# Optimization experiments

Hardware: AMD Instinct MI355X
Metric: run time of the kernel (lower is better)

Reference implementation:

```python
import jax, jax.numpy as jnp
import numpy as np

N = 400000
C_IN = 64
C_OUT = 64
K = 27  # 3x3x3 kernel offsets
EPS = 1e-4


def _subm_conv(feat, nbr_t, W):
    # feat: [N, Cin], nbr_t: [K, N] int32, W: [K, Cin, Cout]
    # rulebook-style gather-GEMM-scatter: accumulate over kernel offsets
    def body(acc, kw):
        Wk, idxk = kw
        return acc + feat[idxk] @ Wk, None
    init = jnp.zeros((feat.shape[0], W.shape[-1]), feat.dtype)
    out, _ = jax.lax.scan(body, init, (W, nbr_t))
    return out


def _bn(x, g, b):
    # BatchNorm1d with track_running_stats=False: always uses batch stats
    m = x.mean(axis=0)
    v = x.var(axis=0)
    return (x - m) * jax.lax.rsqrt(v + EPS) * g + b


def _lrelu(x, slope):
    return jnp.where(x >= 0, x, slope * x)


def setup_inputs() -> dict:
    key = jax.random.key(0)
    ks = jax.random.split(key, 11)
    features = jax.random.normal(ks[0], (N, C_IN), dtype=jnp.float32)
    neighbor_idx = jax.random.randint(ks[1], (N, K), 0, N, dtype=jnp.int32)
    s = 0.05
    W1 = jax.random.normal(ks[2], (K, C_IN, C_OUT), dtype=jnp.float32) * s
    W2 = jax.random.normal(ks[3], (K, C_OUT, C_OUT), dtype=jnp.float32) * s
    W3 = jax.random.normal(ks[4], (K, C_OUT, C_OUT), dtype=jnp.float32) * s
    g1 = jax.random.normal(ks[5], (C_OUT,), dtype=jnp.float32) * 0.1 + 1.0
    b1 = jax.random.normal(ks[6], (C_OUT,), dtype=jnp.float32) * 0.1
    g2 = jax.random.normal(ks[7], (C_OUT,), dtype=jnp.float32) * 0.1 + 1.0
    b2 = jax.random.normal(ks[8], (C_OUT,), dtype=jnp.float32) * 0.1
    g3 = jax.random.normal(ks[9], (C_OUT,), dtype=jnp.float32) * 0.1 + 1.0
    b3 = jax.random.normal(ks[10], (C_OUT,), dtype=jnp.float32) * 0.1
    return {"features": features, "neighbor_idx": neighbor_idx,
            "W1": W1, "g1": g1, "b1": b1,
            "W2": W2, "g2": g2, "b2": b2,
            "W3": W3, "g3": g3, "b3": b3}


def reference(features, neighbor_idx, W1, g1, b1, W2, g2, b2, W3, g3, b3):
    nbr_t = neighbor_idx.T  # [K, N]
    # conv_block1: subm conv -> BN -> LeakyReLU(0.05)
    x = _lrelu(_bn(_subm_conv(features, nbr_t, W1), g1, b1), 0.05)
    res = x
    # conv_block2
    x = _lrelu(_bn(_subm_conv(x, nbr_t, W2), g2, b2), 0.05)
    # conv_block3 (no activation) + norm
    x = _bn(_subm_conv(x, nbr_t, W3), g3, b3)
    # residual add + scn.LeakyReLU (default leakiness = 1/3)
    return _lrelu(x + res, 0.333)
```

## Files before the change

kernel.cpp:

```cpp
#include <hip/hip_runtime.h>
#include <hip/hip_bf16.h>

#define N_PTS 400000
#define KOFF 27
#define AP 72

typedef __attribute__((ext_vector_type(8))) short short8;
typedef __attribute__((ext_vector_type(4))) float float4v;

__device__ __forceinline__ unsigned short f2bf(float f) {
    union { float f; unsigned int u; } a; a.f = f;
    unsigned int u = a.u;
    unsigned int r = (u + 0x7FFFu + ((u >> 16) & 1u)) >> 16;
    return (unsigned short)r;
}

__device__ __forceinline__ float bf2f(unsigned short u) {
    union { unsigned int u; float f; } a; a.u = ((unsigned int)u) << 16;
    return a.f;
}

__global__ void cast_feat_kernel(const float* __restrict__ src,
                                 unsigned short* __restrict__ dst, int n4) {
    int i = blockIdx.x * blockDim.x + threadIdx.x;
    if (i >= n4) return;
    const float4* s4 = (const float4*)src;
    float4 v = s4[i];
    ushort4 o;
    o.x = f2bf(v.x); o.y = f2bf(v.y); o.z = f2bf(v.z); o.w = f2bf(v.w);
    ((ushort4*)dst)[i] = o;
}

__global__ void prep_w_all_kernel(const float* __restrict__ W1,
                                  const float* __restrict__ W2,
                                  const float* __restrict__ W3,
                                  unsigned short* __restrict__ Wt,
                                  float* __restrict__ stats) {
    int i = blockIdx.x * blockDim.x + threadIdx.x;
    if (i < 384) stats[i] = 0.0f;
    if (i >= KOFF * 64 * 64) return;
    int k = i >> 12;
    int co = (i >> 6) & 63;
    int ci = i & 63;
    int src = (k << 12) + (ci << 6) + co;
    const int WS = KOFF * 4096;
    Wt[i] = f2bf(W1[src]);
    Wt[i + WS] = f2bf(W2[src]);
    Wt[i + 2 * WS] = f2bf(W3[src]);
}

__global__ __launch_bounds__(512, 6)
void conv_kernel(const unsigned short* __restrict__ X,
                 const int* __restrict__ nbr,
                 const unsigned short* __restrict__ Wt,
                 float* __restrict__ Y,
                 float* __restrict__ stats) {
    __shared__ unsigned short lds_a[128 * AP];
    __shared__ unsigned short lds_w[64 * AP];
    const int tid = threadIdx.x;
    const int wave = tid >> 6;
    const int lane = tid & 63;
    const int quad = lane >> 4;
    const int l16 = lane & 15;
    const int p0 = blockIdx.x * 128;

    const int sr = tid >> 2;
    const int sq = tid & 3;
    const int wr = tid >> 3;
    const int wc = (tid & 7) << 3;

    float4v acc[4];
    #pragma unroll
    for (int t = 0; t < 4; ++t) acc[t] = (float4v){0.f, 0.f, 0.f, 0.f};

    const long nb = (long)(p0 + sr) * KOFF;
    int gi = nbr[nb];
    int gin = nbr[nb + 1];
    uint4 a0, a1, w0;
    {
        const uint4* srcA = (const uint4*)(X + ((size_t)gi << 6)) + sq * 2;
        a0 = srcA[0];
        a1 = srcA[1];
        w0 = ((const uint4*)Wt)[tid];
    }

    for (int k = 0; k < KOFF; ++k) {
        __syncthreads();
        *(uint4*)(lds_a + sr * AP + sq * 16) = a0;
        *(uint4*)(lds_a + sr * AP + sq * 16 + 8) = a1;
        *(uint4*)(lds_w + wr * AP + wc) = w0;
        if (k < KOFF - 1) {
            const uint4* srcA = (const uint4*)(X + ((size_t)gin << 6)) + sq * 2;
            a0 = srcA[0];
            a1 = srcA[1];
            w0 = ((const uint4*)(Wt + (((size_t)(k + 1)) << 12)))[tid];
            gin = (k < KOFF - 2) ? nbr[nb + k + 2] : 0;
        }
        __syncthreads();
        const int abase = (wave * 16 + l16) * AP + quad * 8;
        #pragma unroll
        for (int ks = 0; ks < 2; ++ks) {
            short8 af = *(const short8*)(lds_a + abase + ks * 32);
            #pragma unroll
            for (int t = 0; t < 4; ++t) {
                short8 bf = *(const short8*)(lds_w + (t * 16 + l16) * AP + ks * 32 + quad * 8);
                acc[t] = __builtin_amdgcn_mfma_f32_16x16x32_bf16(af, bf, acc[t], 0, 0, 0);
            }
        }
    }

    const int row_base = p0 + wave * 16 + quad * 4;
    #pragma unroll
    for (int t = 0; t < 4; ++t) {
        #pragma unroll
        for (int r = 0; r < 4; ++r) {
            Y[(size_t)(row_base + r) * 64 + t * 16 + l16] = acc[t][r];
        }
    }

    __syncthreads();
    float* red = (float*)lds_w;
    if (tid < 128) red[tid] = 0.0f;
    __syncthreads();
    #pragma unroll
    for (int t = 0; t < 4; ++t) {
        float s = acc[t][0] + acc[t][1] + acc[t][2] + acc[t][3];
        float ss = acc[t][0] * acc[t][0] + acc[t][1] * acc[t][1] +
                   acc[t][2] * acc[t][2] + acc[t][3] * acc[t][3];
        s += __shfl_down(s, 32);
        s += __shfl_down(s, 16);
        ss += __shfl_down(ss, 32);
        ss += __shfl_down(ss, 16);
        if (lane < 16) {
            atomicAdd(&red[t * 16 + l16], s);
            atomicAdd(&red[64 + t * 16 + l16], ss);
        }
    }
    __syncthreads();
    if (tid < 128) atomicAdd(&stats[tid], red[tid]);
}

__global__ void bnact_kernel(const float* __restrict__ Y, const float* __restrict__ stats,
                             const float* __restrict__ g, const float* __restrict__ b,
                             unsigned short* __restrict__ Xb, float slope) {
    __shared__ float scale[64], shift[64];
    int tid = threadIdx.x;
    if (tid < 64) {
        float m = stats[tid] * (1.0f / N_PTS);
        float v = stats[64 + tid] * (1.0f / N_PTS) - m * m;
        float rs = rsqrtf(v + 1e-4f);
        float sc = rs * g[tid];
        scale[tid] = sc;
        shift[tid] = b[tid] - m * sc;
    }
    __syncthreads();
    int i = blockIdx.x * blockDim.x + tid;
    const int total = N_PTS * 16;
    if (i >= total) return;
    int cb = (i & 15) << 2;
    float4 y = ((const float4*)Y)[i];
    float o0 = y.x * scale[cb] + shift[cb];
    float o1 = y.y * scale[cb + 1] + shift[cb + 1];
    float o2 = y.z * scale[cb + 2] + shift[cb + 2];
    float o3 = y.w * scale[cb + 3] + shift[cb + 3];
    o0 = o0 >= 0.f ? o0 : slope * o0;
    o1 = o1 >= 0.f ? o1 : slope * o1;
    o2 = o2 >= 0.f ? o2 : slope * o2;
    o3 = o3 >= 0.f ? o3 : slope * o3;
    ushort4 o;
    o.x = f2bf(o0); o.y = f2bf(o1); o.z = f2bf(o2); o.w = f2bf(o3);
    ((ushort4*)Xb)[i] = o;
}

__global__ void bnact_final_kernel(float* __restrict__ Y, const float* __restrict__ stats,
                                   const float* __restrict__ g, const float* __restrict__ b,
                                   const unsigned short* __restrict__ res) {
    __shared__ float scale[64], shift[64];
    int tid = threadIdx.x;
    if (tid < 64) {
        float m = stats[tid] * (1.0f / N_PTS);
        float v = stats[64 + tid] * (1.0f / N_PTS) - m * m;
        float rs = rsqrtf(v + 1e-4f);
        float sc = rs * g[tid];
        scale[tid] = sc;
        shift[tid] = b[tid] - m * sc;
    }
    __syncthreads();
    int i = blockIdx.x * blockDim.x + tid;
    const int total = N_PTS * 16;
    if (i >= total) return;
    int cb = (i & 15) << 2;
    float4 y = ((const float4*)Y)[i];
    ushort4 r4 = ((const ushort4*)res)[i];
    float o0 = y.x * scale[cb] + shift[cb] + bf2f(r4.x);
    float o1 = y.y * scale[cb + 1] + shift[cb + 1] + bf2f(r4.y);
    float o2 = y.z * scale[cb + 2] + shift[cb + 2] + bf2f(r4.z);
    float o3 = y.w * scale[cb + 3] + shift[cb + 3] + bf2f(r4.w);
    o0 = o0 >= 0.f ? o0 : 0.333f * o0;
    o1 = o1 >= 0.f ? o1 : 0.333f * o1;
    o2 = o2 >= 0.f ? o2 : 0.333f * o2;
    o3 = o3 >= 0.f ? o3 : 0.333f * o3;
    float4 o; o.x = o0; o.y = o1; o.z = o2; o.w = o3;
    ((float4*)Y)[i] = o;
}

extern "C" void kernel_launch(void* const* d_in, const int* in_sizes, int n_in,
                              void* d_out, int out_size, void* d_ws, size_t ws_size,
                              hipStream_t stream) {
    const float* feat = (const float*)d_in[0];
    const int* nbr = (const int*)d_in[1];
    const float* W1 = (const float*)d_in[2];
    const float* g1 = (const float*)d_in[3];
    const float* b1 = (const float*)d_in[4];
    const float* W2 = (const float*)d_in[5];
    const float* g2 = (const float*)d_in[6];
    const float* b2 = (const float*)d_in[7];
    const float* W3 = (const float*)d_in[8];
    const float* g3 = (const float*)d_in[9];
    const float* b3 = (const float*)d_in[10];
    float* Y = (float*)d_out;

    char* ws = (char*)d_ws;
    const size_t BF_BYTES = (size_t)N_PTS * 64 * 2;
    unsigned short* B0 = (unsigned short*)ws;
    unsigned short* B1 = (unsigned short*)(ws + BF_BYTES);
    unsigned short* Wt = (unsigned short*)(ws + 2 * BF_BYTES);
    float* stats = (float*)(ws + 2 * BF_BYTES + (size_t)3 * KOFF * 4096 * 2);

    const int WSTRIDE = KOFF * 4096;

    cast_feat_kernel<<<25000, 256, 0, stream>>>(feat, B0, N_PTS * 16);
    prep_w_all_kernel<<<(KOFF * 4096 + 255) / 256, 256, 0, stream>>>(W1, W2, W3, Wt, stats);

    conv_kernel<<<N_PTS / 128, 512, 0, stream>>>(B0, nbr, Wt, Y, stats);
    bnact_kernel<<<25000, 256, 0, stream>>>(Y, stats, g1, b1, B1, 0.05f);
    conv_kernel<<<N_PTS / 128, 512, 0, stream>>>(B1, nbr, Wt + WSTRIDE, Y, stats + 128);
    bnact_kernel<<<25000, 256, 0, stream>>>(Y, stats + 128, g2, b2, B0, 0.05f);
    conv_kernel<<<N_PTS / 128, 512, 0, stream>>>(B0, nbr, Wt + 2 * WSTRIDE, Y, stats + 256);
    bnact_final_kernel<<<25000, 256, 0, stream>>>(Y, stats + 256, g3, b3, B1);
}
```

Before: 1.001 ms.

## Load gathered A fragments directly into registers and double-buffer weight tiles

The conv kernel no longer stages gathered neighbor rows through LDS. Each lane loads its MFMA A-fragments straight from global memory into registers. Each wave now covers 32 rows (two M tiles) with 256 threads per block, so every B fragment read from LDS is reused across two MFMA row tiles. Weights are double-buffered in LDS with one barrier per kernel offset instead of two. The cost is higher register pressure and fewer threads per block to hide gather latency.

New measurement: 1.042 ms. 4.1% more time.

```diff
diff --git a/kernel.cpp b/kernel.cpp
--- a/kernel.cpp
+++ b/kernel.cpp
@@ -49,84 +49,110 @@
     Wt[i + 2 * WS] = f2bf(W3[src]);
 }
 
-__global__ __launch_bounds__(512, 6)
+__global__ __launch_bounds__(256, 4)
 void conv_kernel(const unsigned short* __restrict__ X,
                  const int* __restrict__ nbr,
                  const unsigned short* __restrict__ Wt,
                  float* __restrict__ Y,
                  float* __restrict__ stats) {
-    __shared__ unsigned short lds_a[128 * AP];
-    __shared__ unsigned short lds_w[64 * AP];
+    __shared__ unsigned short lds_w[2][64 * AP];
     const int tid = threadIdx.x;
     const int wave = tid >> 6;
     const int lane = tid & 63;
     const int quad = lane >> 4;
     const int l16 = lane & 15;
     const int p0 = blockIdx.x * 128;
-
-    const int sr = tid >> 2;
-    const int sq = tid & 3;
-    const int wr = tid >> 3;
-    const int wc = (tid & 7) << 3;
-
-    float4v acc[4];
+    const char* Xb = (const char*)X;
+
+    const long nb0 = (long)(p0 + wave * 32 + l16) * KOFF;
+    const long nb1 = nb0 + 16 * KOFF;
+
+    const int wrow = tid >> 3;
+    const int wcol = (tid & 7) << 3;
+    const int wrow2 = (tid + 256) >> 3;
+
+    float4v acc[2][4];
     #pragma unroll
-    for (int t = 0; t < 4; ++t) acc[t] = (float4v){0.f, 0.f, 0.f, 0.f};
-
-    const long nb = (long)(p0 + sr) * KOFF;
-    int gi = nbr[nb];
-    int gin = nbr[nb + 1];
-    uint4 a0, a1, w0;
-    {
-        const uint4* srcA = (const uint4*)(X + ((size_t)gi << 6)) + sq * 2;
-        a0 = srcA[0];
-        a1 = srcA[1];
-        w0 = ((const uint4*)Wt)[tid];
-    }
+    for (int mt = 0; mt < 2; ++mt)
+        #pragma unroll
+        for (int t = 0; t < 4; ++t) acc[mt][t] = (float4v){0.f, 0.f, 0.f, 0.f};
+
+    int i0 = nbr[nb0] << 7;
+    int i1 = nbr[nb1] << 7;
+    uint4 w0 = ((const uint4*)Wt)[tid];
+    uint4 w1 = ((const uint4*)Wt)[tid + 256];
+    short8 a00 = *(const short8*)(Xb + i0 + quad * 16);
+    short8 a01 = *(const short8*)(Xb + i0 + quad * 16 + 64);
+    short8 a10 = *(const short8*)(Xb + i1 + quad * 16);
+    short8 a11 = *(const short8*)(Xb + i1 + quad * 16 + 64);
+    *(uint4*)(&lds_w[0][wrow * AP + wcol]) = w0;
+    *(uint4*)(&lds_w[0][wrow2 * AP + wcol]) = w1;
+    int j0 = nbr[nb0 + 1] << 7;
+    int j1 = nbr[nb1 + 1] << 7;
+    __syncthreads();
 
     for (int k = 0; k < KOFF; ++k) {
+        const int cb = k & 1;
+        short8 n00, n01, n10, n11;
+        uint4 v0, v1;
+        if (k < KOFF - 1) {
+            const uint4* Wk = (const uint4*)(Wt + (((size_t)(k + 1)) << 12));
+            v0 = Wk[tid];
+            v1 = Wk[tid + 256];
+            n00 = *(const short8*)(Xb + j0 + quad * 16);
+            n01 = *(const short8*)(Xb + j0 + quad * 16 + 64);
+            n10 = *(const short8*)(Xb + j1 + quad * 16);
+            n11 = *(const short8*)(Xb + j1 + quad * 16 + 64);
+        }
+        if (k < KOFF - 2) {
+            j0 = nbr[nb0 + k + 2] << 7;
+            j1 = nbr[nb1 + k + 2] << 7;
+        }
+        #pragma unroll
+        for (int t = 0; t < 4; ++t) {
+            short8 b0 = *(const short8*)(&lds_w[cb][(t * 16 + l16) * AP + quad * 8]);
+            short8 b1 = *(const short8*)(&lds_w[cb][(t * 16 + l16) * AP + 32 + quad * 8]);
+            acc[0][t] = __builtin_amdgcn_mfma_f32_16x16x32_bf16(a00, b0, acc[0][t], 0, 0, 0);
+            acc[0][t] = __builtin_amdgcn_mfma_f32_16x16x32_bf16(a01, b1, acc[0][t], 0, 0, 0);
+            acc[1][t] = __builtin_amdgcn_mfma_f32_16x16x32_bf16(a10, b0, acc[1][t], 0, 0, 0);
+            acc[1][t] = __builtin_amdgcn_mfma_f32_16x16x32_bf16(a11, b1, acc[1][t], 0, 0, 0);
+        }
+        if (k < KOFF - 1) {
+            const int nbuf = cb ^ 1;
+            *(uint4*)(&lds_w[nbuf][wrow * AP + wcol]) = v0;
+            *(uint4*)(&lds_w[nbuf][wrow2 * AP + wcol]) = v1;
+            a00 = n00; a01 = n01; a10 = n10; a11 = n11;
+        }
         __syncthreads();
-        *(uint4*)(lds_a + sr * AP + sq * 16) = a0;
-        *(uint4*)(lds_a + sr * AP + sq * 16 + 8) = a1;
-        *(uint4*)(lds_w + wr * AP + wc) = w0;
-        if (k < KOFF - 1) {
-            const uint4* srcA = (const uint4*)(X + ((size_t)gin << 6)) + sq * 2;
-            a0 = srcA[0];
-            a1 = srcA[1];
-            w0 = ((const uint4*)(Wt + (((size_t)(k + 1)) << 12)))[tid];
-            gin = (k < KOFF - 2) ? nbr[nb + k + 2] : 0;
-        }
-        __syncthreads();
-        const int abase = (wave * 16 + l16) * AP + quad * 8;
-        #pragma unroll
-        for (int ks = 0; ks < 2; ++ks) {
-            short8 af = *(const short8*)(lds_a + abase + ks * 32);
+    }
+
+    const int rb = p0 + wave * 32 + quad * 4;
+    #pragma unroll
+    for (int mt = 0; mt < 2; ++mt) {
+        #pragma unroll
+        for (int t = 0; t < 4; ++t) {
             #pragma unroll
-            for (int t = 0; t < 4; ++t) {
-                short8 bf = *(const short8*)(lds_w + (t * 16 + l16) * AP + ks * 32 + quad * 8);
-                acc[t] = __builtin_amdgcn_mfma_f32_16x16x32_bf16(af, bf, acc[t], 0, 0, 0);
+            for (int r = 0; r < 4; ++r) {
+                Y[(size_t)(rb + mt * 16 + r) * 64 + t * 16 + l16] = acc[mt][t][r];
             }
         }
     }
 
-    const int row_base = p0 + wave * 16 + quad * 4;
+    float* red = (float*)lds_w;
+    if (tid < 128) red[tid] = 0.0f;
+    __syncthreads();
     #pragma unroll
     for (int t = 0; t < 4; ++t) {
-        #pragma unroll
-        for (int r = 0; r < 4; ++r) {
-            Y[(size_t)(row_base + r) * 64 + t * 16 + l16] = acc[t][r];
-        }
-    }
-
-    __syncthreads();
-    float* red = (float*)lds_w;
-    if (tid < 128) red[tid] = 0.0f;
-    __syncthreads();
-    #pragma unroll
-    for (int t = 0; t < 4; ++t) {
-        float s = acc[t][0] + acc[t][1] + acc[t][2] + acc[t][3];
-        float ss = acc[t][0] * acc[t][0] + acc[t][1] * acc[t][1] +
-                   acc[t][2] * acc[t][2] + acc[t][3] * acc[t][3];
+        float s = 0.f, ss = 0.f;
+        #pragma unroll
+        for (int mt = 0; mt < 2; ++mt) {
+            #pragma unroll
+            for (int r = 0; r < 4; ++r) {
+                float v = acc[mt][t][r];
+                s += v;
+                ss += v * v;
+            }
+        }
         s += __shfl_down(s, 32);
         s += __shfl_down(s, 16);
         ss += __shfl_down(ss, 32);
@@ -232,10 +258,10 @@
     cast_feat_kernel<<<25000, 256, 0, stream>>>(feat, B0, N_PTS * 16);
     prep_w_all_kernel<<<(KOFF * 4096 + 255) / 256, 256, 0, stream>>>(W1, W2, W3, Wt, stats);
 
-    conv_kernel<<<N_PTS / 128, 512, 0, stream>>>(B0, nbr, Wt, Y, stats);
+    conv_kernel<<<N_PTS / 128, 256, 0, stream>>>(B0, nbr, Wt, Y, stats);
     bnact_kernel<<<25000, 256, 0, stream>>>(Y, stats, g1, b1, B1, 0.05f);
-    conv_kernel<<<N_PTS / 128, 512, 0, stream>>>(B1, nbr, Wt + WSTRIDE, Y, stats + 128);
+    conv_kernel<<<N_PTS / 128, 256, 0, stream>>>(B1, nbr, Wt + WSTRIDE, Y, stats + 128);
     bnact_kernel<<<25000, 256, 0, stream>>>(Y, stats + 128, g2, b2, B0, 0.05f);
-    conv_kernel<<<N_PTS / 128, 512, 0, stream>>>(B0, nbr, Wt + 2 * WSTRIDE, Y, stats + 256);
+    conv_kernel<<<N_PTS / 128, 256, 0, stream>>>(B0, nbr, Wt + 2 * WSTRIDE, Y, stats + 256);
     bnact_final_kernel<<<25000, 256, 0, stream>>>(Y, stats + 256, g3, b3, B1);
 }
```
